# Kernel optimization log

Hardware: AMD Instinct MI355X
Metric: run time of the kernel (lower is better)

The kernel has to match this reference:

```python
import jax, jax.numpy as jnp
import numpy as np

B, N, D = 4, 4096, 256

def setup_inputs() -> dict:
    key = jax.random.key(0)
    k1, = jax.random.split(key, 1)
    x = jax.random.normal(k1, (B, N, D), dtype=jnp.float32)
    attn_mask = jnp.ones((B, 1, N), dtype=jnp.int32)
    pad_mask = jnp.ones((B, 1, N), dtype=jnp.int32)
    return {"x": x, "attn_mask": attn_mask, "pad_mask": pad_mask, "dim_": D}

def reference(x, attn_mask, pad_mask, dim_):
    # adj is None -> scores = x @ x^T / sqrt(d)
    scale = jnp.sqrt(jnp.asarray(x.shape[-1], x.dtype))
    scores = jnp.einsum('bnd,bmd->bnm', x, x) / scale  # [B, N, N]
    # NOTE: original calls non-in-place masked_fill and discards the result,
    # so pad_mask / attn_mask have no effect on the output (faithful).
    prob = jax.nn.softmax(scores, axis=-1)
    # dropout is identity in inference mode
    return jnp.einsum('bnm,bmd->bnd', prob, x)
```

## Files before the change

kernel.cpp:

```cpp
#include <hip/hip_runtime.h>

typedef __attribute__((ext_vector_type(8))) short short8;
typedef __attribute__((ext_vector_type(4))) float f32x4;
typedef __attribute__((ext_vector_type(4))) unsigned int u32x4;

#define NTOK 4096
#define DIM  256
#define P_STRIDE 72
#define TILE_ELEMS 32768

__device__ __forceinline__ unsigned pack2bf(float a, float b) {
  unsigned ua = __builtin_bit_cast(unsigned, a) + 0x8000u;
  unsigned ub = __builtin_bit_cast(unsigned, b) + 0x8000u;
  return __builtin_amdgcn_perm(ub, ua, 0x07060302u);
}

__global__ __launch_bounds__(256, 4)
void prep_kernel(const float* __restrict__ X, unsigned short* __restrict__ Img) {
  __shared__ __align__(16) unsigned short rowbf[8 * 256];
  const int b    = blockIdx.x & 3;
  const int sub  = blockIdx.x >> 2;
  const int t    = sub >> 3;
  const int part = sub & 7;
  const int tid  = threadIdx.x;
  const float* src = X + ((size_t)b * NTOK + t * 64 + part * 8) * DIM;
  unsigned short* dst = Img + ((size_t)(b * 64 + t)) * TILE_ELEMS;
  {
    const int r = tid >> 5;
    const int c = tid & 31;
    const float* s = src + r * DIM + c * 8;
    f32x4 f0 = *(const f32x4*)s;
    f32x4 f1 = *(const f32x4*)(s + 4);
    union { unsigned u[4]; u32x4 v; } p;
    p.u[0] = pack2bf(f0[0], f0[1]);
    p.u[1] = pack2bf(f0[2], f0[3]);
    p.u[2] = pack2bf(f1[0], f1[1]);
    p.u[3] = pack2bf(f1[2], f1[3]);
    const int gr = part * 8 + r;
    *(u32x4*)(dst + gr * 256 + ((c ^ (gr & 7)) << 3)) = p.v;
    *(u32x4*)(&rowbf[r * 256 + c * 8]) = p.v;
  }
  __syncthreads();
  {
    const int d = tid;
    union { unsigned short s[8]; u32x4 v; } p;
    #pragma unroll
    for (int i = 0; i < 8; ++i) p.s[i] = rowbf[i * 256 + d];
    *(u32x4*)(dst + 16384 + part * 2048 + d * 8) = p.v;
  }
}

#define FA_STEP(T, VLD, VUS)                                                   \
  {                                                                            \
    const int t_ = (T);                                                        \
    __syncthreads();            \
    const int buf_ = t_ & 1;                                                   \
    if (!isQK) {                                                               \
      {                                                                        \
        const unsigned short* vt = vtg + (size_t)t_ * TILE_ELEMS;              \
        _Pragma("unroll")                                                      \
        for (int ks = 0; ks < 2; ++ks)                                         \
          _Pragma("unroll")                                                    \
          for (int dt = 0; dt < 4; ++dt)                                       \
            u[(VLD) + ks * 4 + dt] = __builtin_bit_cast(f32x4,                 \
                *(const short8*)(vt + (ks * 4 + quad) * 2048 + dt * 128));     \
      }                                                                        \
      if (t_ > 0) {                                                            \
        const unsigned short* prd = pb[buf_ ^ 1];                              \
        __builtin_amdgcn_s_setprio(1);                                         \
        _Pragma("unroll")                                                      \
        for (int ks = 0; ks < 2; ++ks) {                                       \
          const int pos = (ks * 4 + quad) ^ ((ln >> 3) << 1);                  \
          _Pragma("unroll")                                                    \
          for (int s = 0; s < 4; ++s) {                                        \
            short8 ap = *(const short8*)(                                      \
                &prd[(s * 16 + ln) * P_STRIDE + (pos << 3)]);                  \
            _Pragma("unroll")                                                  \
            for (int dt = 0; dt < 4; ++dt)                                     \
              u[s * 4 + dt] = __builtin_amdgcn_mfma_f32_16x16x32_bf16(         \
                  ap, __builtin_bit_cast(short8, u[(VUS) + ks * 4 + dt]),      \
                  u[s * 4 + dt], 0, 0, 0);                                     \
          }                                                                    \
        }                                                                      \
        __builtin_amdgcn_s_setprio(0);                                         \
      }                                                                        \
    } else {                                                                   \
                    \
      const unsigned short* kR =                                               \
          imgb + (size_t)t_ * TILE_ELEMS + (role * 16 + ln) * 256;             \
      short8 bk[8];                                                            \
      _Pragma("unroll")                                                        \
      for (int ds = 0; ds < 8; ++ds)                                           \
        bk[ds] = *(const short8*)(kR + (((ds * 4 + quad) ^ swz) << 3));        \
      f32x4 sf[4];                                                             \
      _Pragma("unroll")                                                        \
      for (int s = 0; s < 4; ++s) sf[s] = (f32x4)(0.0f);                       \
      __builtin_amdgcn_s_setprio(1);                                           \
      _Pragma("unroll")                                                        \
      for (int ds = 0; ds < 8; ++ds)                                           \
        _Pragma("unroll")                                                      \
        for (int s = 0; s < 4; ++s)                                            \
          sf[s] = __builtin_amdgcn_mfma_f32_16x16x32_bf16(                     \
              __builtin_bit_cast(short8, u[s * 8 + ds]), bk[ds], sf[s],        \
              0, 0, 0);                                                        \
      __builtin_amdgcn_s_setprio(0);                                           \
      unsigned short* pw = pb[buf_];                                           \
      _Pragma("unroll")                                                        \
      for (int s = 0; s < 4; ++s) {                                            \
        unsigned pd[4];                                                        \
        _Pragma("unroll")                                                      \
        for (int j = 0; j < 4; ++j) {                                          \
          float p0 = __builtin_amdgcn_exp2f(sf[s][j] * c2);                    \
          lrow[s][j] += p0;                                                    \
          unsigned q0 = __builtin_bit_cast(unsigned, p0);                      \
          unsigned n0 = (unsigned)__builtin_amdgcn_mov_dpp((int)q0, 0xB1,      \
                                                           0xF, 0xF, true);   \
          pd[j] = pack2bf(p0, __builtin_bit_cast(float, n0));                  \
        }                                                                      \
        if ((ln & 1) == 0) {                                                   \
          _Pragma("unroll")                                                    \
          for (int j = 0; j < 4; ++j)                                          \
            *(unsigned*)(&pw[(s * 16 + quad * 4 + j) * P_STRIDE +              \
                             pwPos + pwCol]) = pd[j];                          \
        }                                                                      \
      }                                                                        \
    }                                                                          \
  }

__global__ __launch_bounds__(512, 1)
void fa_kernel(const unsigned short* __restrict__ Img, float* __restrict__ Out) {
  __shared__ __align__(16) unsigned short pb[2][64 * P_STRIDE];
  __shared__ float lbuf[64][4];

  const int tid  = threadIdx.x;
  const int b    = blockIdx.x & 3;
  const int qblk = blockIdx.x >> 2;
  const int wave = tid >> 6;
  const int lane = tid & 63;
  const int ln   = lane & 15;
  const int quad = lane >> 4;
  const int swz  = ln & 7;
  const bool isQK = wave < 4;
  const int  role = wave & 3;

  const unsigned short* imgb = Img + (size_t)b * 64 * TILE_ELEMS;

  const float c2 = 0.0901684400f;

  const int pwPos = ((role * 2 + (ln >> 3)) ^ ((quad >> 1) << 1)) << 3;
  const int pwCol = ln & 7;

  const unsigned short* vtg = imgb + 16384 + (size_t)(role * 64 + ln) * 8;

  float lrow[4][4] = {{0,0,0,0},{0,0,0,0},{0,0,0,0},{0,0,0,0}};

  f32x4 u[32];
  if (isQK) {
    #pragma unroll
    for (int s = 0; s < 4; ++s) {
      const unsigned short* qrow =
          imgb + (size_t)qblk * TILE_ELEMS + (s * 16 + ln) * 256;
      #pragma unroll
      for (int ds = 0; ds < 8; ++ds)
        u[s * 8 + ds] = __builtin_bit_cast(f32x4,
            *(const short8*)(qrow + (((ds * 4 + quad) ^ swz) << 3)));
    }
  } else {
    #pragma unroll
    for (int i = 0; i < 16; ++i) u[i] = (f32x4)(0.0f);
  }

  FA_STEP(0, 16, 24);
  #pragma unroll 1
  for (int tt = 1; tt < 63; tt += 2) {
    FA_STEP(tt, 24, 16);
    FA_STEP(tt + 1, 16, 24);
  }
  FA_STEP(63, 24, 16);

  __syncthreads();

  if (isQK) {
    #pragma unroll
    for (int off = 1; off < 16; off <<= 1)
      #pragma unroll
      for (int s = 0; s < 4; ++s)
        #pragma unroll
        for (int j = 0; j < 4; ++j)
          lrow[s][j] += __shfl_xor(lrow[s][j], off, 64);
    if (ln == 0) {
      #pragma unroll
      for (int s = 0; s < 4; ++s)
        #pragma unroll
        for (int j = 0; j < 4; ++j)
          lbuf[s * 16 + quad * 4 + j][role] = lrow[s][j];
    }
  } else {
    const unsigned short* prd = pb[1];
    #pragma unroll
    for (int ks = 0; ks < 2; ++ks) {
      const int pos = (ks * 4 + quad) ^ ((ln >> 3) << 1);
      #pragma unroll
      for (int s = 0; s < 4; ++s) {
        short8 ap = *(const short8*)(&prd[(s * 16 + ln) * P_STRIDE + (pos << 3)]);
        #pragma unroll
        for (int dt = 0; dt < 4; ++dt)
          u[s * 4 + dt] = __builtin_amdgcn_mfma_f32_16x16x32_bf16(
              ap, __builtin_bit_cast(short8, u[24 + ks * 4 + dt]),
              u[s * 4 + dt], 0, 0, 0);
      }
    }
  }
  __syncthreads();

  if (!isQK) {
    float* outB = Out + (size_t)(b * NTOK + qblk * 64) * DIM + role * 64;
    #pragma unroll
    for (int s = 0; s < 4; ++s) {
      #pragma unroll
      for (int j = 0; j < 4; ++j) {
        const int row = s * 16 + quad * 4 + j;
        f32x4 lv = *(const f32x4*)lbuf[row];
        const float rl = 1.0f / (lv[0] + lv[1] + lv[2] + lv[3]);
        #pragma unroll
        for (int dt = 0; dt < 4; ++dt)
          outB[(size_t)row * DIM + dt * 16 + ln] = u[s * 4 + dt][j] * rl;
      }
    }
  }
}

extern "C" void kernel_launch(void* const* d_in, const int* in_sizes, int n_in,
                              void* d_out, int out_size, void* d_ws, size_t ws_size,
                              hipStream_t stream) {
  const float* X = (const float*)d_in[0];
  float* Out = (float*)d_out;
  unsigned short* Img = (unsigned short*)d_ws;
  (void)in_sizes; (void)n_in; (void)out_size; (void)ws_size;
  hipLaunchKernelGGL(prep_kernel, dim3(2048), dim3(256), 0, stream, X, Img);
  hipLaunchKernelGGL(fa_kernel, dim3(256), dim3(512), 0, stream, Img, Out);
}
```

Measured before the change: 163.8 us.

## Deepen software pipeline by deferring exp/store and PV by one extra step

```diff
diff --git a/kernel.cpp b/kernel.cpp
--- a/kernel.cpp
+++ b/kernel.cpp
@@ -50,80 +50,69 @@
   }
 }
 
-#define FA_STEP(T, VLD, VUS)                                                   \
+#define PV_TAIL(PRD, SB)                                                       \
+  {                                                                            \
+    const unsigned short* prd = (PRD);                                         \
+    _Pragma("unroll")                                                          \
+    for (int ks = 0; ks < 2; ++ks) {                                           \
+      const int pos = (ks * 4 + quad) ^ ((ln >> 3) << 1);                      \
+      _Pragma("unroll")                                                        \
+      for (int s = 0; s < 4; ++s) {                                            \
+        short8 ap = *(const short8*)(&prd[(s * 16 + ln) * P_STRIDE +           \
+                                          (pos << 3)]);                        \
+        _Pragma("unroll")                                                      \
+        for (int dt = 0; dt < 4; ++dt)                                         \
+          u[s * 4 + dt] = __builtin_amdgcn_mfma_f32_16x16x32_bf16(             \
+              ap, __builtin_bit_cast(short8, u[(SB) + ks * 4 + dt]),           \
+              u[s * 4 + dt], 0, 0, 0);                                         \
+      }                                                                        \
+    }                                                                          \
+  }
+
+#define FA_STEP(T, SETB)                                                       \
   {                                                                            \
     const int t_ = (T);                                                        \
-    __syncthreads();            \
-    const int buf_ = t_ & 1;                                                   \
+    __syncthreads();         \
     if (!isQK) {                                                               \
-      {                                                                        \
+      if (t_ > 1) {                                                            \
+        __builtin_amdgcn_s_setprio(1);                                         \
+        PV_TAIL(pb[t_ & 1], SETB);                        \
+        __builtin_amdgcn_s_setprio(0);                                         \
+      }                                                                        \
+      {          \
         const unsigned short* vt = vtg + (size_t)t_ * TILE_ELEMS;              \
         _Pragma("unroll")                                                      \
         for (int ks = 0; ks < 2; ++ks)                                         \
           _Pragma("unroll")                                                    \
           for (int dt = 0; dt < 4; ++dt)                                       \
-            u[(VLD) + ks * 4 + dt] = __builtin_bit_cast(f32x4,                 \
+            u[(SETB) + ks * 4 + dt] = __builtin_bit_cast(f32x4,                \
                 *(const short8*)(vt + (ks * 4 + quad) * 2048 + dt * 128));     \
       }                                                                        \
-      if (t_ > 0) {                                                            \
-        const unsigned short* prd = pb[buf_ ^ 1];                              \
-        __builtin_amdgcn_s_setprio(1);                                         \
-        _Pragma("unroll")                                                      \
-        for (int ks = 0; ks < 2; ++ks) {                                       \
-          const int pos = (ks * 4 + quad) ^ ((ln >> 3) << 1);                  \
-          _Pragma("unroll")                                                    \
-          for (int s = 0; s < 4; ++s) {                                        \
-            short8 ap = *(const short8*)(                                      \
-                &prd[(s * 16 + ln) * P_STRIDE + (pos << 3)]);                  \
-            _Pragma("unroll")                                                  \
-            for (int dt = 0; dt < 4; ++dt)                                     \
-              u[s * 4 + dt] = __builtin_amdgcn_mfma_f32_16x16x32_bf16(         \
-                  ap, __builtin_bit_cast(short8, u[(VUS) + ks * 4 + dt]),      \
-                  u[s * 4 + dt], 0, 0, 0);                                     \
-          }                                                                    \
-        }                                                                      \
-        __builtin_amdgcn_s_setprio(0);                                         \
-      }                                                                        \
     } else {                                                                   \
-                    \
+                                             \
       const unsigned short* kR =                                               \
           imgb + (size_t)t_ * TILE_ELEMS + (role * 16 + ln) * 256;             \
       short8 bk[8];                                                            \
       _Pragma("unroll")                                                        \
       for (int ds = 0; ds < 8; ++ds)                                           \
         bk[ds] = *(const short8*)(kR + (((ds * 4 + quad) ^ swz) << 3));        \
-      f32x4 sf[4];                                                             \
-      _Pragma("unroll")                                                        \
-      for (int s = 0; s < 4; ++s) sf[s] = (f32x4)(0.0f);                       \
+          \
+      if (t_ > 0) expstore((t_ & 1) ^ 1);                                      \
+                          \
       __builtin_amdgcn_s_setprio(1);                                           \
       _Pragma("unroll")                                                        \
-      for (int ds = 0; ds < 8; ++ds)                                           \
+      for (int s = 0; s < 4; ++s)                                              \
+        sfo[s] = __builtin_amdgcn_mfma_f32_16x16x32_bf16(                      \
+            __builtin_bit_cast(short8, u[s * 8]), bk[0], (f32x4)(0.0f),        \
+            0, 0, 0);                                                          \
+      _Pragma("unroll")                                                        \
+      for (int ds = 1; ds < 8; ++ds)                                           \
         _Pragma("unroll")                                                      \
         for (int s = 0; s < 4; ++s)                                            \
-          sf[s] = __builtin_amdgcn_mfma_f32_16x16x32_bf16(                     \
-              __builtin_bit_cast(short8, u[s * 8 + ds]), bk[ds], sf[s],        \
+          sfo[s] = __builtin_amdgcn_mfma_f32_16x16x32_bf16(                    \
+              __builtin_bit_cast(short8, u[s * 8 + ds]), bk[ds], sfo[s],       \
               0, 0, 0);                                                        \
       __builtin_amdgcn_s_setprio(0);                                           \
-      unsigned short* pw = pb[buf_];                                           \
-      _Pragma("unroll")                                                        \
-      for (int s = 0; s < 4; ++s) {                                            \
-        unsigned pd[4];                                                        \
-        _Pragma("unroll")                                                      \
-        for (int j = 0; j < 4; ++j) {                                          \
-          float p0 = __builtin_amdgcn_exp2f(sf[s][j] * c2);                    \
-          lrow[s][j] += p0;                                                    \
-          unsigned q0 = __builtin_bit_cast(unsigned, p0);                      \
-          unsigned n0 = (unsigned)__builtin_amdgcn_mov_dpp((int)q0, 0xB1,      \
-                                                           0xF, 0xF, true);   \
-          pd[j] = pack2bf(p0, __builtin_bit_cast(float, n0));                  \
-        }                                                                      \
-        if ((ln & 1) == 0) {                                                   \
-          _Pragma("unroll")                                                    \
-          for (int j = 0; j < 4; ++j)                                          \
-            *(unsigned*)(&pw[(s * 16 + quad * 4 + j) * P_STRIDE +              \
-                             pwPos + pwCol]) = pd[j];                          \
-        }                                                                      \
-      }                                                                        \
     }                                                                          \
   }
 
@@ -153,6 +142,7 @@
   const unsigned short* vtg = imgb + 16384 + (size_t)(role * 64 + ln) * 8;
 
   float lrow[4][4] = {{0,0,0,0},{0,0,0,0},{0,0,0,0},{0,0,0,0}};
+  f32x4 sfo[4];
 
   f32x4 u[32];
   if (isQK) {
@@ -170,14 +160,41 @@
     for (int i = 0; i < 16; ++i) u[i] = (f32x4)(0.0f);
   }
 
-  FA_STEP(0, 16, 24);
+  auto expstore = [&](int pwbuf) __attribute__((always_inline)) {
+    unsigned short* pw = pb[pwbuf];
+    #pragma unroll
+    for (int s = 0; s < 4; ++s) {
+      unsigned pd[4];
+      #pragma unroll
+      for (int j = 0; j < 4; ++j) {
+        float p0 = __builtin_amdgcn_exp2f(sfo[s][j] * c2);
+        lrow[s][j] += p0;
+        unsigned q0 = __builtin_bit_cast(unsigned, p0);
+        unsigned n0 = (unsigned)__builtin_amdgcn_mov_dpp((int)q0, 0xB1,
+                                                         0xF, 0xF, true);
+        pd[j] = pack2bf(p0, __builtin_bit_cast(float, n0));
+      }
+      if ((ln & 1) == 0) {
+        #pragma unroll
+        for (int j = 0; j < 4; ++j)
+          *(unsigned*)(&pw[(s * 16 + quad * 4 + j) * P_STRIDE +
+                           pwPos + pwCol]) = pd[j];
+      }
+    }
+  };
+
   #pragma unroll 1
-  for (int tt = 1; tt < 63; tt += 2) {
-    FA_STEP(tt, 24, 16);
-    FA_STEP(tt + 1, 16, 24);
-  }
-  FA_STEP(63, 24, 16);
-
+  for (int tt = 0; tt < 64; tt += 2) {
+    FA_STEP(tt, 16);
+    FA_STEP(tt + 1, 24);
+  }
+
+  __syncthreads();
+  if (isQK) {
+    expstore(1);
+  } else {
+    PV_TAIL(pb[0], 16);
+  }
   __syncthreads();
 
   if (isQK) {
@@ -196,20 +213,7 @@
           lbuf[s * 16 + quad * 4 + j][role] = lrow[s][j];
     }
   } else {
-    const unsigned short* prd = pb[1];
-    #pragma unroll
-    for (int ks = 0; ks < 2; ++ks) {
-      const int pos = (ks * 4 + quad) ^ ((ln >> 3) << 1);
-      #pragma unroll
-      for (int s = 0; s < 4; ++s) {
-        short8 ap = *(const short8*)(&prd[(s * 16 + ln) * P_STRIDE + (pos << 3)]);
-        #pragma unroll
-        for (int dt = 0; dt < 4; ++dt)
-          u[s * 4 + dt] = __builtin_amdgcn_mfma_f32_16x16x32_bf16(
-              ap, __builtin_bit_cast(short8, u[24 + ks * 4 + dt]),
-              u[s * 4 + dt], 0, 0, 0);
-      }
-    }
+    PV_TAIL(pb[1], 24);
   }
   __syncthreads();
 
```

Result: faster. 144.1 us (-12.0%).
